# Kernel tuning notes

Measured on AMD Instinct MI355X. Metric: run time of the kernel, lower is better.

The kernel has to match this reference:

```python
import jax, jax.numpy as jnp
import numpy as np

N_NODES = 50000


def gcn_conv(x, W, b, src, dst, n_nodes):
    # PyG GCNConv: y = D^-1/2 (A + I) D^-1/2 (x @ W) + b, with D counting self-loops
    h = x @ W                                             # [N, out]
    deg = jnp.ones((n_nodes,), h.dtype).at[dst].add(1.0)  # in-degree + self-loop
    dinv = jax.lax.rsqrt(deg)
    norm = dinv[src] * dinv[dst]                          # [E]
    msg = h[src] * norm[:, None]                          # [E, out]
    out = jnp.zeros_like(h).at[dst].add(msg)              # scatter-add over edges
    out = out + h * (dinv * dinv)[:, None]                # self-loop contribution
    return out + b


def setup_inputs() -> dict:
    key = jax.random.key(0)
    k = jax.random.split(key, 7)
    d_in, d_hid, d_out = 128, 128, 64
    x = jax.random.normal(k[0], (N_NODES, d_in), jnp.float32)
    edge_index = jax.random.randint(k[1], (2, 800000), 0, N_NODES, jnp.int64)
    s1 = 1.0 / np.sqrt(d_in)
    s2 = 1.0 / np.sqrt(d_hid)
    W1 = jax.random.uniform(k[2], (d_in, d_hid), jnp.float32, -s1, s1)
    b1 = jnp.zeros((d_hid,), jnp.float32)
    W2 = jax.random.uniform(k[3], (d_hid, d_out), jnp.float32, -s2, s2)
    b2 = jnp.zeros((d_out,), jnp.float32)
    return {"x": x, "edge_index": edge_index, "W1": W1, "b1": b1, "W2": W2, "b2": b2}


def reference(x, edge_index, W1, b1, W2, b2):
    src, dst = edge_index[0], edge_index[1]
    h = jax.nn.relu(gcn_conv(x, W1, b1, src, dst, N_NODES))
    h = gcn_conv(h, W2, b2, src, dst, N_NODES)
    return jax.nn.log_softmax(h, axis=1)
```

## Files before the change

kernel.cpp:

```cpp
#include <hip/hip_runtime.h>
#include <hip/hip_bf16.h>
#include <math.h>


typedef unsigned int uint32;
typedef unsigned short ushort16;
typedef __attribute__((ext_vector_type(8))) short bf16x8;
typedef __attribute__((ext_vector_type(4))) float f32x4;

__device__ inline unsigned short f2bf_rne(float f) {
    uint32 x = __float_as_uint(f);
    uint32 r = (x + 0x7fffu + ((x >> 16) & 1u)) >> 16;
    return (unsigned short)r;
}
__device__ inline uint32 pack_bf16x2(float a, float b) {
    return (uint32)f2bf_rne(a) | ((uint32)f2bf_rne(b) << 16);
}
__device__ inline float2 unpack_bf16x2(uint32 u) {
    float2 r;
    r.x = __uint_as_float(u << 16);
    r.y = __uint_as_float(u & 0xffff0000u);
    return r;
}

#define NHB 128

__global__ __launch_bounds__(256) void hist_conv_k(const int* __restrict__ dst, int E,
                                                   int NW, int chunk,
                                                   uint32* __restrict__ counts_pb,
                                                   ushort16* __restrict__ rankx,
                                                   const float* __restrict__ W1,
                                                   const float* __restrict__ W2,
                                                   unsigned short* __restrict__ W1t,
                                                   unsigned short* __restrict__ W2t) {
    const int tid = threadIdx.x;
    if ((int)blockIdx.x >= 4 * NHB) {
        int idx = ((int)blockIdx.x - 4 * NHB) * 256 + tid;
        if (idx < 128 * 128) {
            int ns = idx >> 7, k = idx & 127;
            int t = ns >> 4, m = ns & 15;
            int col = 32 * (t >> 1) + 2 * m + (t & 1);
            W1t[idx] = f2bf_rne(W1[k * 128 + col]);
        } else {
            int i2 = idx - 128 * 128;
            if (i2 < 64 * 128) {
                int ns = i2 >> 7, k = i2 & 127;
                int t = ns >> 4, m = ns & 15;
                int col = 32 * (t >> 1) + 2 * m + (t & 1);
                W2t[i2] = f2bf_rne(W2[k * 64 + col]);
            }
        }
        return;
    }
    extern __shared__ uint32 sh[];
    const int hb  = blockIdx.x >> 2;
    const int qt  = blockIdx.x & 3;
    const int NWq = (NW + 3) >> 2;
    const int qlo = qt * NWq;
    const int qhi = min(NW, qlo + NWq);
    const int qn  = qhi - qlo;
    for (int i = tid; i < qn; i += 256) sh[i] = 0;
    __syncthreads();
    const int e0 = hb * chunk;
    const int e1 = min(E, e0 + chunk);
    int e = e0 + tid;
    for (; e + 768 < e1; e += 1024) {
        int d0 = dst[e];
        int d1 = dst[e + 256];
        int d2 = dst[e + 512];
        int d3 = dst[e + 768];
        int w0 = d0 >> 1, w1 = d1 >> 1, w2 = d2 >> 1, w3 = d3 >> 1;
        if (w0 >= qlo && w0 < qhi) {
            uint32 o = atomicAdd(&sh[w0 - qlo], (d0 & 1) ? 0x10000u : 1u);
            rankx[e] = (ushort16)((d0 & 1) ? (o >> 16) : (o & 0xffffu));
        }
        if (w1 >= qlo && w1 < qhi) {
            uint32 o = atomicAdd(&sh[w1 - qlo], (d1 & 1) ? 0x10000u : 1u);
            rankx[e + 256] = (ushort16)((d1 & 1) ? (o >> 16) : (o & 0xffffu));
        }
        if (w2 >= qlo && w2 < qhi) {
            uint32 o = atomicAdd(&sh[w2 - qlo], (d2 & 1) ? 0x10000u : 1u);
            rankx[e + 512] = (ushort16)((d2 & 1) ? (o >> 16) : (o & 0xffffu));
        }
        if (w3 >= qlo && w3 < qhi) {
            uint32 o = atomicAdd(&sh[w3 - qlo], (d3 & 1) ? 0x10000u : 1u);
            rankx[e + 768] = (ushort16)((d3 & 1) ? (o >> 16) : (o & 0xffffu));
        }
    }
    for (; e < e1; e += 256) {
        int d = dst[e];
        int w = d >> 1;
        if (w >= qlo && w < qhi) {
            uint32 o = atomicAdd(&sh[w - qlo], (d & 1) ? 0x10000u : 1u);
            rankx[e] = (ushort16)((d & 1) ? (o >> 16) : (o & 0xffffu));
        }
    }
    __syncthreads();
    uint32* dstp = counts_pb + (size_t)hb * NW + qlo;
    for (int i = tid; i < qn; i += 256) dstp[i] = sh[i];
}

__global__ __launch_bounds__(256) void scan2_k(const uint32* __restrict__ counts_pb,
                                               int N, int NW,
                                               ushort16* __restrict__ basecum,
                                               int* __restrict__ exscan,
                                               int* __restrict__ blocksum,
                                               float* __restrict__ dinv,
                                               ushort16* __restrict__ degs) {
    __shared__ int sd[256];
    const int tid = threadIdx.x;
    const int n   = blockIdx.x * 256 + tid;
    const int nc  = n < N ? n : N - 1;
    const int w   = nc >> 1;
    const bool hi = (nc & 1) != 0;
    int cum = 0;
    for (int bb = 0; bb < NHB; bb += 16) {
        uint32 wv[16];
#pragma unroll
        for (int j = 0; j < 16; ++j)
            wv[j] = counts_pb[(size_t)(bb + j) * NW + w];
#pragma unroll
        for (int j = 0; j < 16; ++j) {
            int c = hi ? (int)(wv[j] >> 16) : (int)(wv[j] & 0xffffu);
            if (n < N) basecum[(size_t)(bb + j) * N + n] = (ushort16)cum;
            cum += c;
        }
    }
    int v = (n < N) ? cum : 0;
    if (n < N) {
        dinv[n] = rsqrtf((float)(v + 1));
        degs[n] = (ushort16)v;
    }
    int vp = (v + 7) & ~7;
    sd[tid] = vp;
    __syncthreads();
    for (int off = 1; off < 256; off <<= 1) {
        int t = (tid >= off) ? sd[tid - off] : 0;
        __syncthreads();
        sd[tid] += t;
        __syncthreads();
    }
    if (n < N) exscan[n] = sd[tid] - vp;
    if (tid == 255) blocksum[blockIdx.x] = sd[255];
}

__global__ __launch_bounds__(256) void fill_gemm1_k(const int* __restrict__ src,
                                                    const int* __restrict__ dst, int E,
                                                    int chunk, int N,
                                                    const ushort16* __restrict__ rankx,
                                                    const ushort16* __restrict__ basecum,
                                                    const int* __restrict__ blocksum,
                                                    int NB,
                                                    const int* __restrict__ exscan,
                                                    const ushort16* __restrict__ degs,
                                                    int* __restrict__ offsets,
                                                    ushort16* __restrict__ csr_src,
                                                    const float* __restrict__ X,
                                                    const unsigned short* __restrict__ Wt,
                                                    const float* __restrict__ dinv,
                                                    uint32* __restrict__ Yu, int Nrows) {
    __shared__ int sd[256];
    __shared__ int ebs[256];
    __shared__ int total;
    if ((int)blockIdx.x < 256) {
        const int f   = blockIdx.x;
        const int tid = threadIdx.x;
        int v = (tid < NB) ? blocksum[tid] : 0;
        sd[tid] = v;
        __syncthreads();
        for (int off = 1; off < 256; off <<= 1) {
            int t = (tid >= off) ? sd[tid - off] : 0;
            __syncthreads();
            sd[tid] += t;
            __syncthreads();
        }
        ebs[tid] = sd[tid] - v;
        if (tid == 255) total = sd[255];
        __syncthreads();
        int g = f * 256 + tid;
        if (g < N) {
            int off = ebs[g >> 8] + exscan[g];
            offsets[g] = off;
            int dg = degs[g];
            int pl = (dg + 7) & ~7;
            for (int k = dg; k < pl; ++k) csr_src[off + k] = (ushort16)N;
        } else if (g == N) {
            offsets[N] = total;
        }
        const int b  = f >> 1;
        const ushort16* bc = basecum + (size_t)b * N;
        const int q2 = chunk >> 1;
        const int e0 = b * chunk + (f & 1) * q2;
        const int e1 = min(E, e0 + q2);
        int e = e0 + tid;
        for (; e + 768 < e1; e += 1024) {
#pragma unroll
            for (int j = 0; j < 4; ++j) {
                int ej = e + j * 256;
                int d = dst[ej];
                int pos = ebs[d >> 8] + exscan[d] + (int)bc[d] + (int)rankx[ej];
                csr_src[pos] = (ushort16)src[ej];
            }
        }
        for (; e < e1; e += 256) {
            int d = dst[e];
            int pos = ebs[d >> 8] + exscan[d] + (int)bc[d] + (int)rankx[e];
            csr_src[pos] = (ushort16)src[e];
        }
        return;
    }
    constexpr int NCOL = 128;
    constexpr int NT = NCOL / 16;
    const int tid  = threadIdx.x;
    const int wave = tid >> 6;
    const int lane = tid & 63;
    const int m16  = lane & 15;
    const int q    = lane >> 4;
    const int r0   = ((int)blockIdx.x - 256) * 64 + wave * 16;

    if ((int)blockIdx.x == 256 && tid < 64) Yu[(size_t)Nrows * (NCOL / 2) + tid] = 0;

    int arow = r0 + m16;
    if (arow >= Nrows) arow = Nrows - 1;

    bf16x8 afrag[4];
#pragma unroll
    for (int kb = 0; kb < 4; ++kb) {
        const float* p = &X[(size_t)arow * 128 + kb * 32 + q * 8];
        float4 u0 = *(const float4*)p;
        float4 u1 = *(const float4*)(p + 4);
        bf16x8 a;
        a[0] = (short)f2bf_rne(u0.x); a[1] = (short)f2bf_rne(u0.y);
        a[2] = (short)f2bf_rne(u0.z); a[3] = (short)f2bf_rne(u0.w);
        a[4] = (short)f2bf_rne(u1.x); a[5] = (short)f2bf_rne(u1.y);
        a[6] = (short)f2bf_rne(u1.z); a[7] = (short)f2bf_rne(u1.w);
        afrag[kb] = a;
    }

    f32x4 acc[NT];
#pragma unroll
    for (int t = 0; t < NT; ++t) acc[t] = (f32x4){0.f, 0.f, 0.f, 0.f};
#pragma unroll
    for (int t = 0; t < NT; ++t) {
        const unsigned short* Bp = &Wt[(size_t)(t * 16 + m16) * 128 + q * 8];
#pragma unroll
        for (int kb = 0; kb < 4; ++kb) {
            bf16x8 bfrag = *(const bf16x8*)&Bp[kb * 32];
            acc[t] = __builtin_amdgcn_mfma_f32_16x16x32_bf16(afrag[kb], bfrag, acc[t], 0, 0, 0);
        }
    }
#pragma unroll
    for (int i = 0; i < 4; ++i) {
        int row = r0 + q * 4 + i;
        if (row < Nrows) {
            float dn = dinv[row];
#pragma unroll
            for (int u = 0; u < NT / 2; ++u)
                Yu[(size_t)row * (NCOL / 2) + u * 16 + m16] =
                    pack_bf16x2(acc[2 * u][i] * dn, acc[2 * u + 1][i] * dn);
        }
    }
}

__global__ __launch_bounds__(256, 8) void agg1_gemm2_k(const unsigned short* __restrict__ hs,
                                                       const int* __restrict__ offsets,
                                                       const ushort16* __restrict__ csr_src,
                                                       const float* __restrict__ dinv,
                                                       const float* __restrict__ b1,
                                                       const unsigned short* __restrict__ W2t,
                                                       uint32* __restrict__ Yu, int N) {
    __shared__ uint32 srow[16 * 68];
    const int tid  = threadIdx.x;
    const int w    = tid >> 6;
    const int lane = tid & 63;
    const int base = (int)blockIdx.x * 16;
    const uint32* T = (const uint32*)hs;
    const float2 bb = ((const float2*)b1)[lane];
    if (blockIdx.x == 0 && w == 2 && lane < 32) Yu[(size_t)N * 32 + lane] = 0;
#pragma unroll
    for (int which = 0; which < 4; ++which) {
        const int node = base + 4 * w + which;
        uint32 packed = 0;
        if (node < N) {
            const int start = offsets[node];
            const int end   = offsets[node + 1];
            const float dn  = dinv[node];
            float2 self = unpack_bf16x2(T[(size_t)node * 64 + lane]);
            float ax0 = self.x, ay0 = self.y;
            float ax1 = 0.f, ay1 = 0.f, ax2 = 0.f, ay2 = 0.f, ax3 = 0.f, ay3 = 0.f;
            int p = start;
            for (; p + 15 < end; p += 16) {
                uint4 ia = *(const uint4*)&csr_src[p];
                uint4 ib = *(const uint4*)&csr_src[p + 8];
                int s0 = ia.x & 0xffff, s1 = ia.x >> 16;
                int s2 = ia.y & 0xffff, s3 = ia.y >> 16;
                int s4 = ia.z & 0xffff, s5 = ia.z >> 16;
                int s6 = ia.w & 0xffff, s7 = ia.w >> 16;
                int s8 = ib.x & 0xffff, s9 = ib.x >> 16;
                int sa = ib.y & 0xffff, sb = ib.y >> 16;
                int sc = ib.z & 0xffff, sd = ib.z >> 16;
                int se = ib.w & 0xffff, sf = ib.w >> 16;
                uint32 u0 = T[(size_t)s0 * 64 + lane];
                uint32 u1 = T[(size_t)s1 * 64 + lane];
                uint32 u2 = T[(size_t)s2 * 64 + lane];
                uint32 u3 = T[(size_t)s3 * 64 + lane];
                uint32 u4 = T[(size_t)s4 * 64 + lane];
                uint32 u5 = T[(size_t)s5 * 64 + lane];
                uint32 u6 = T[(size_t)s6 * 64 + lane];
                uint32 u7 = T[(size_t)s7 * 64 + lane];
                uint32 u8 = T[(size_t)s8 * 64 + lane];
                uint32 u9 = T[(size_t)s9 * 64 + lane];
                uint32 ua = T[(size_t)sa * 64 + lane];
                uint32 ub = T[(size_t)sb * 64 + lane];
                uint32 uc = T[(size_t)sc * 64 + lane];
                uint32 ud = T[(size_t)sd * 64 + lane];
                uint32 ue = T[(size_t)se * 64 + lane];
                uint32 uf = T[(size_t)sf * 64 + lane];
                float2 f0 = unpack_bf16x2(u0), f1 = unpack_bf16x2(u1);
                float2 f2 = unpack_bf16x2(u2), f3 = unpack_bf16x2(u3);
                float2 f4 = unpack_bf16x2(u4), f5 = unpack_bf16x2(u5);
                float2 f6 = unpack_bf16x2(u6), f7 = unpack_bf16x2(u7);
                float2 f8 = unpack_bf16x2(u8), f9 = unpack_bf16x2(u9);
                float2 fa = unpack_bf16x2(ua), fb = unpack_bf16x2(ub);
                float2 fc = unpack_bf16x2(uc), fd = unpack_bf16x2(ud);
                float2 fe = unpack_bf16x2(ue), ff = unpack_bf16x2(uf);
                ax0 += (f0.x + f4.x) + (f8.x + fc.x);
                ay0 += (f0.y + f4.y) + (f8.y + fc.y);
                ax1 += (f1.x + f5.x) + (f9.x + fd.x);
                ay1 += (f1.y + f5.y) + (f9.y + fd.y);
                ax2 += (f2.x + f6.x) + (fa.x + fe.x);
                ay2 += (f2.y + f6.y) + (fa.y + fe.y);
                ax3 += (f3.x + f7.x) + (fb.x + ff.x);
                ay3 += (f3.y + f7.y) + (fb.y + ff.y);
            }
            for (; p + 7 < end; p += 8) {
                uint4 ia = *(const uint4*)&csr_src[p];
                int s0 = ia.x & 0xffff, s1 = ia.x >> 16;
                int s2 = ia.y & 0xffff, s3 = ia.y >> 16;
                int s4 = ia.z & 0xffff, s5 = ia.z >> 16;
                int s6 = ia.w & 0xffff, s7 = ia.w >> 16;
                uint32 u0 = T[(size_t)s0 * 64 + lane];
                uint32 u1 = T[(size_t)s1 * 64 + lane];
                uint32 u2 = T[(size_t)s2 * 64 + lane];
                uint32 u3 = T[(size_t)s3 * 64 + lane];
                uint32 u4 = T[(size_t)s4 * 64 + lane];
                uint32 u5 = T[(size_t)s5 * 64 + lane];
                uint32 u6 = T[(size_t)s6 * 64 + lane];
                uint32 u7 = T[(size_t)s7 * 64 + lane];
                float2 f0 = unpack_bf16x2(u0), f1 = unpack_bf16x2(u1);
                float2 f2 = unpack_bf16x2(u2), f3 = unpack_bf16x2(u3);
                float2 f4 = unpack_bf16x2(u4), f5 = unpack_bf16x2(u5);
                float2 f6 = unpack_bf16x2(u6), f7 = unpack_bf16x2(u7);
                ax0 += f0.x + f4.x; ay0 += f0.y + f4.y;
                ax1 += f1.x + f5.x; ay1 += f1.y + f5.y;
                ax2 += f2.x + f6.x; ay2 += f2.y + f6.y;
                ax3 += f3.x + f7.x; ay3 += f3.y + f7.y;
            }
            float vx = ((ax0 + ax1) + (ax2 + ax3)) * dn + bb.x;
            float vy = ((ay0 + ay1) + (ay2 + ay3)) * dn + bb.y;
            vx = vx > 0.f ? vx : 0.f;
            vy = vy > 0.f ? vy : 0.f;
            packed = pack_bf16x2(vx, vy);
        }
        srow[(4 * w + which) * 68 + lane] = packed;
    }
    __syncthreads();
    if (w < 2) {
        const int pp  = w;
        const int m16 = lane & 15;
        const int q   = lane >> 4;
        bf16x8 afrag[4];
#pragma unroll
        for (int kb = 0; kb < 4; ++kb)
            afrag[kb] = *(const bf16x8*)&srow[m16 * 68 + kb * 16 + q * 4];
        f32x4 acc0 = (f32x4){0.f, 0.f, 0.f, 0.f};
        f32x4 acc1 = (f32x4){0.f, 0.f, 0.f, 0.f};
        const unsigned short* Bp0 = &W2t[(size_t)((2 * pp) * 16 + m16) * 128 + q * 8];
        const unsigned short* Bp1 = &W2t[(size_t)((2 * pp + 1) * 16 + m16) * 128 + q * 8];
#pragma unroll
        for (int kb = 0; kb < 4; ++kb) {
            bf16x8 b0  = *(const bf16x8*)&Bp0[kb * 32];
            bf16x8 b1f = *(const bf16x8*)&Bp1[kb * 32];
            acc0 = __builtin_amdgcn_mfma_f32_16x16x32_bf16(afrag[kb], b0, acc0, 0, 0, 0);
            acc1 = __builtin_amdgcn_mfma_f32_16x16x32_bf16(afrag[kb], b1f, acc1, 0, 0, 0);
        }
#pragma unroll
        for (int i = 0; i < 4; ++i) {
            int row = base + q * 4 + i;
            if (row < N) {
                float dn2 = dinv[row];
                Yu[(size_t)row * 32 + pp * 16 + m16] =
                    pack_bf16x2(acc0[i] * dn2, acc1[i] * dn2);
            }
        }
    }
}

__global__ __launch_bounds__(256, 8) void agg2_k(const unsigned short* __restrict__ hs,
                                                 const int* __restrict__ offsets,
                                                 const ushort16* __restrict__ csr_src,
                                                 const float* __restrict__ dinv,
                                                 const float* __restrict__ b2,
                                                 float* __restrict__ out, int N) {
    const int tid  = threadIdx.x;
    const int node = blockIdx.x * 8 + (tid >> 5);
    const int l    = tid & 31;
    if (node >= N) return;
    const uint32* T = (const uint32*)hs;
    const int start = offsets[node];
    const int end   = offsets[node + 1];
    const float dn  = dinv[node];
    float2 self = unpack_bf16x2(T[(size_t)node * 32 + l]);
    float ax0 = self.x, ay0 = self.y;
    float ax1 = 0.f, ay1 = 0.f, ax2 = 0.f, ay2 = 0.f, ax3 = 0.f, ay3 = 0.f;
    int p = start;
    for (; p + 15 < end; p += 16) {
        uint4 ia = *(const uint4*)&csr_src[p];
        uint4 ib = *(const uint4*)&csr_src[p + 8];
        int s0 = ia.x & 0xffff, s1 = ia.x >> 16;
        int s2 = ia.y & 0xffff, s3 = ia.y >> 16;
        int s4 = ia.z & 0xffff, s5 = ia.z >> 16;
        int s6 = ia.w & 0xffff, s7 = ia.w >> 16;
        int s8 = ib.x & 0xffff, s9 = ib.x >> 16;
        int sa = ib.y & 0xffff, sb = ib.y >> 16;
        int sc = ib.z & 0xffff, sd = ib.z >> 16;
        int se = ib.w & 0xffff, sf = ib.w >> 16;
        uint32 u0 = T[(size_t)s0 * 32 + l];
        uint32 u1 = T[(size_t)s1 * 32 + l];
        uint32 u2 = T[(size_t)s2 * 32 + l];
        uint32 u3 = T[(size_t)s3 * 32 + l];
        uint32 u4 = T[(size_t)s4 * 32 + l];
        uint32 u5 = T[(size_t)s5 * 32 + l];
        uint32 u6 = T[(size_t)s6 * 32 + l];
        uint32 u7 = T[(size_t)s7 * 32 + l];
        uint32 u8 = T[(size_t)s8 * 32 + l];
        uint32 u9 = T[(size_t)s9 * 32 + l];
        uint32 ua = T[(size_t)sa * 32 + l];
        uint32 ub = T[(size_t)sb * 32 + l];
        uint32 uc = T[(size_t)sc * 32 + l];
        uint32 ud = T[(size_t)sd * 32 + l];
        uint32 ue = T[(size_t)se * 32 + l];
        uint32 uf = T[(size_t)sf * 32 + l];
        float2 f0 = unpack_bf16x2(u0), f1 = unpack_bf16x2(u1);
        float2 f2 = unpack_bf16x2(u2), f3 = unpack_bf16x2(u3);
        float2 f4 = unpack_bf16x2(u4), f5 = unpack_bf16x2(u5);
        float2 f6 = unpack_bf16x2(u6), f7 = unpack_bf16x2(u7);
        float2 f8 = unpack_bf16x2(u8), f9 = unpack_bf16x2(u9);
        float2 fa = unpack_bf16x2(ua), fb = unpack_bf16x2(ub);
        float2 fc = unpack_bf16x2(uc), fd = unpack_bf16x2(ud);
        float2 fe = unpack_bf16x2(ue), ff = unpack_bf16x2(uf);
        ax0 += (f0.x + f4.x) + (f8.x + fc.x);
        ay0 += (f0.y + f4.y) + (f8.y + fc.y);
        ax1 += (f1.x + f5.x) + (f9.x + fd.x);
        ay1 += (f1.y + f5.y) + (f9.y + fd.y);
        ax2 += (f2.x + f6.x) + (fa.x + fe.x);
        ay2 += (f2.y + f6.y) + (fa.y + fe.y);
        ax3 += (f3.x + f7.x) + (fb.x + ff.x);
        ay3 += (f3.y + f7.y) + (fb.y + ff.y);
    }
    for (; p + 7 < end; p += 8) {
        uint4 ia = *(const uint4*)&csr_src[p];
        int s0 = ia.x & 0xffff, s1 = ia.x >> 16;
        int s2 = ia.y & 0xffff, s3 = ia.y >> 16;
        int s4 = ia.z & 0xffff, s5 = ia.z >> 16;
        int s6 = ia.w & 0xffff, s7 = ia.w >> 16;
        uint32 u0 = T[(size_t)s0 * 32 + l];
        uint32 u1 = T[(size_t)s1 * 32 + l];
        uint32 u2 = T[(size_t)s2 * 32 + l];
        uint32 u3 = T[(size_t)s3 * 32 + l];
        uint32 u4 = T[(size_t)s4 * 32 + l];
        uint32 u5 = T[(size_t)s5 * 32 + l];
        uint32 u6 = T[(size_t)s6 * 32 + l];
        uint32 u7 = T[(size_t)s7 * 32 + l];
        float2 f0 = unpack_bf16x2(u0), f1 = unpack_bf16x2(u1);
        float2 f2 = unpack_bf16x2(u2), f3 = unpack_bf16x2(u3);
        float2 f4 = unpack_bf16x2(u4), f5 = unpack_bf16x2(u5);
        float2 f6 = unpack_bf16x2(u6), f7 = unpack_bf16x2(u7);
        ax0 += f0.x + f4.x; ay0 += f0.y + f4.y;
        ax1 += f1.x + f5.x; ay1 += f1.y + f5.y;
        ax2 += f2.x + f6.x; ay2 += f2.y + f6.y;
        ax3 += f3.x + f7.x; ay3 += f3.y + f7.y;
    }
    float2 bb = ((const float2*)b2)[l];
    float vx = ((ax0 + ax1) + (ax2 + ax3)) * dn + bb.x;
    float vy = ((ay0 + ay1) + (ay2 + ay3)) * dn + bb.y;
    float m = fmaxf(vx, vy);
#pragma unroll
    for (int off = 16; off > 0; off >>= 1) m = fmaxf(m, __shfl_xor(m, off, 64));
    float ex = __expf(vx - m) + __expf(vy - m);
    float ssum = ex;
#pragma unroll
    for (int off = 16; off > 0; off >>= 1) ssum += __shfl_xor(ssum, off, 64);
    float lse = m + __logf(ssum);
    float2 o = {vx - lse, vy - lse};
    ((float2*)out)[(size_t)node * 32 + l] = o;
}

extern "C" void kernel_launch(void* const* d_in, const int* in_sizes, int n_in,
                              void* d_out, int out_size, void* d_ws, size_t ws_size,
                              hipStream_t stream) {
    const float* x  = (const float*)d_in[0];
    const int*   ei = (const int*)d_in[1];
    const float* W1 = (const float*)d_in[2];
    const float* b1 = (const float*)d_in[3];
    const float* W2 = (const float*)d_in[4];
    const float* b2 = (const float*)d_in[5];
    float* out = (float*)d_out;

    const int N = in_sizes[0] / 128;
    const int E = in_sizes[1] / 2;
    const int* src = ei;
    const int* dst = ei + E;
    const int NB = (N + 255) / 256;
    const int NW = (N + 1) / 2;
    const int NWq = (NW + 3) >> 2;
    const int chunk = (E + NHB - 1) / NHB;

    char* ws = (char*)d_ws;
    auto alloc = [&](size_t bytes) -> char* {
        char* p = ws;
        ws += (bytes + 255) & ~(size_t)255;
        return p;
    };
    unsigned short* h1  = (unsigned short*)alloc((size_t)(N + 1) * 128 * 2);
    unsigned short* h2  = (unsigned short*)alloc((size_t)(N + 1) * 64 * 2);
    uint32* counts_pb = (uint32*)alloc((size_t)NHB * NW * 4);
    ushort16* basecum = (ushort16*)alloc((size_t)NHB * N * 2);
    ushort16* rankx   = (ushort16*)alloc((size_t)E * 2);
    ushort16* csr_src = (ushort16*)alloc(((size_t)E + 8 * (size_t)N) * 2);
    float* dinv     = (float*)alloc((size_t)N * 4);
    int*   exscan   = (int*)alloc((size_t)N * 4);
    int*   blocksum = (int*)alloc((size_t)NB * 4);
    int*   offsets  = (int*)alloc((size_t)(N + 1) * 4);
    ushort16* degs  = (ushort16*)alloc((size_t)N * 2);
    unsigned short* W1t = (unsigned short*)alloc(128 * 128 * 2);
    unsigned short* W2t = (unsigned short*)alloc(64 * 128 * 2);

    const int GB = (N + 63) / 64;
    const int CB = (128 * 128 + 64 * 128 + 255) / 256;

    hist_conv_k<<<4 * NHB + CB, 256, NWq * 4, stream>>>(dst, E, NW, chunk, counts_pb,
                                                        rankx, W1, W2, W1t, W2t);
    scan2_k<<<NB, 256, 0, stream>>>(counts_pb, N, NW, basecum, exscan, blocksum, dinv,
                                    degs);
    fill_gemm1_k<<<256 + GB, 256, 0, stream>>>(src, dst, E, chunk, N, rankx, basecum,
                                               blocksum, NB, exscan, degs, offsets,
                                               csr_src, x, W1t, dinv, (uint32*)h1, N);
    agg1_gemm2_k<<<(N + 15) / 16, 256, 0, stream>>>(h1, offsets, csr_src, dinv, b1,
                                                    W2t, (uint32*)h2, N);
    agg2_k<<<(N + 7) / 8, 256, 0, stream>>>(h2, offsets, csr_src, dinv, b2, out, N);
}
```

Before: 180.0 us.

## Pack CSR-build counters into 8-bit fields and split agg2 edges across half-waves

The histogram now packs four 8-bit per-node counters into each shared-memory word instead of two 16-bit ones. This shrinks counts_pb, and stores rankx and basecum as bytes, which cuts memory traffic in the hist, scan and fill kernels. The final aggregation kernel now gives each node a full 64-lane wave and splits its edge list between the two 32-lane halves, combining them with a shuffle. This adds parallelism per node but drops the 16-wide unrolled path. The 8-bit counters assume that per-node degree, and its running sum across histogram blocks, stays below 256; larger degrees would overflow silently.

```diff
diff --git a/kernel.cpp b/kernel.cpp
--- a/kernel.cpp
+++ b/kernel.cpp
@@ -5,6 +5,7 @@
 
 typedef unsigned int uint32;
 typedef unsigned short ushort16;
+typedef unsigned char uchar;
 typedef __attribute__((ext_vector_type(8))) short bf16x8;
 typedef __attribute__((ext_vector_type(4))) float f32x4;
 
@@ -26,9 +27,9 @@
 #define NHB 128
 
 __global__ __launch_bounds__(256) void hist_conv_k(const int* __restrict__ dst, int E,
-                                                   int NW, int chunk,
+                                                   int NWb, int chunk,
                                                    uint32* __restrict__ counts_pb,
-                                                   ushort16* __restrict__ rankx,
+                                                   uchar* __restrict__ rankx,
                                                    const float* __restrict__ W1,
                                                    const float* __restrict__ W2,
                                                    unsigned short* __restrict__ W1t,
@@ -55,9 +56,9 @@
     extern __shared__ uint32 sh[];
     const int hb  = blockIdx.x >> 2;
     const int qt  = blockIdx.x & 3;
-    const int NWq = (NW + 3) >> 2;
+    const int NWq = (NWb + 3) >> 2;
     const int qlo = qt * NWq;
-    const int qhi = min(NW, qlo + NWq);
+    const int qhi = min(NWb, qlo + NWq);
     const int qn  = qhi - qlo;
     for (int i = tid; i < qn; i += 256) sh[i] = 0;
     __syncthreads();
@@ -69,40 +70,40 @@
         int d1 = dst[e + 256];
         int d2 = dst[e + 512];
         int d3 = dst[e + 768];
-        int w0 = d0 >> 1, w1 = d1 >> 1, w2 = d2 >> 1, w3 = d3 >> 1;
+        int w0 = d0 >> 2, w1 = d1 >> 2, w2 = d2 >> 2, w3 = d3 >> 2;
         if (w0 >= qlo && w0 < qhi) {
-            uint32 o = atomicAdd(&sh[w0 - qlo], (d0 & 1) ? 0x10000u : 1u);
-            rankx[e] = (ushort16)((d0 & 1) ? (o >> 16) : (o & 0xffffu));
+            uint32 o = atomicAdd(&sh[w0 - qlo], 1u << (8 * (d0 & 3)));
+            rankx[e] = (uchar)(o >> (8 * (d0 & 3)));
         }
         if (w1 >= qlo && w1 < qhi) {
-            uint32 o = atomicAdd(&sh[w1 - qlo], (d1 & 1) ? 0x10000u : 1u);
-            rankx[e + 256] = (ushort16)((d1 & 1) ? (o >> 16) : (o & 0xffffu));
+            uint32 o = atomicAdd(&sh[w1 - qlo], 1u << (8 * (d1 & 3)));
+            rankx[e + 256] = (uchar)(o >> (8 * (d1 & 3)));
         }
         if (w2 >= qlo && w2 < qhi) {
-            uint32 o = atomicAdd(&sh[w2 - qlo], (d2 & 1) ? 0x10000u : 1u);
-            rankx[e + 512] = (ushort16)((d2 & 1) ? (o >> 16) : (o & 0xffffu));
+            uint32 o = atomicAdd(&sh[w2 - qlo], 1u << (8 * (d2 & 3)));
+            rankx[e + 512] = (uchar)(o >> (8 * (d2 & 3)));
         }
         if (w3 >= qlo && w3 < qhi) {
-            uint32 o = atomicAdd(&sh[w3 - qlo], (d3 & 1) ? 0x10000u : 1u);
-            rankx[e + 768] = (ushort16)((d3 & 1) ? (o >> 16) : (o & 0xffffu));
+            uint32 o = atomicAdd(&sh[w3 - qlo], 1u << (8 * (d3 & 3)));
+            rankx[e + 768] = (uchar)(o >> (8 * (d3 & 3)));
         }
     }
     for (; e < e1; e += 256) {
         int d = dst[e];
-        int w = d >> 1;
+        int w = d >> 2;
         if (w >= qlo && w < qhi) {
-            uint32 o = atomicAdd(&sh[w - qlo], (d & 1) ? 0x10000u : 1u);
-            rankx[e] = (ushort16)((d & 1) ? (o >> 16) : (o & 0xffffu));
+            uint32 o = atomicAdd(&sh[w - qlo], 1u << (8 * (d & 3)));
+            rankx[e] = (uchar)(o >> (8 * (d & 3)));
         }
     }
     __syncthreads();
-    uint32* dstp = counts_pb + (size_t)hb * NW + qlo;
+    uint32* dstp = counts_pb + (size_t)hb * NWb + qlo;
     for (int i = tid; i < qn; i += 256) dstp[i] = sh[i];
 }
 
 __global__ __launch_bounds__(256) void scan2_k(const uint32* __restrict__ counts_pb,
-                                               int N, int NW,
-                                               ushort16* __restrict__ basecum,
+                                               int N, int NWb,
+                                               uchar* __restrict__ basecum,
                                                int* __restrict__ exscan,
                                                int* __restrict__ blocksum,
                                                float* __restrict__ dinv,
@@ -111,18 +112,18 @@
     const int tid = threadIdx.x;
     const int n   = blockIdx.x * 256 + tid;
     const int nc  = n < N ? n : N - 1;
-    const int w   = nc >> 1;
-    const bool hi = (nc & 1) != 0;
+    const int wq  = nc >> 2;
+    const int sh8 = 8 * (nc & 3);
     int cum = 0;
     for (int bb = 0; bb < NHB; bb += 16) {
         uint32 wv[16];
 #pragma unroll
         for (int j = 0; j < 16; ++j)
-            wv[j] = counts_pb[(size_t)(bb + j) * NW + w];
+            wv[j] = counts_pb[(size_t)(bb + j) * NWb + wq];
 #pragma unroll
         for (int j = 0; j < 16; ++j) {
-            int c = hi ? (int)(wv[j] >> 16) : (int)(wv[j] & 0xffffu);
-            if (n < N) basecum[(size_t)(bb + j) * N + n] = (ushort16)cum;
+            int c = (int)((wv[j] >> sh8) & 0xffu);
+            if (n < N) basecum[(size_t)(bb + j) * N + n] = (uchar)cum;
             cum += c;
         }
     }
@@ -147,8 +148,8 @@
 __global__ __launch_bounds__(256) void fill_gemm1_k(const int* __restrict__ src,
                                                     const int* __restrict__ dst, int E,
                                                     int chunk, int N,
-                                                    const ushort16* __restrict__ rankx,
-                                                    const ushort16* __restrict__ basecum,
+                                                    const uchar* __restrict__ rankx,
+                                                    const uchar* __restrict__ basecum,
                                                     const int* __restrict__ blocksum,
                                                     int NB,
                                                     const int* __restrict__ exscan,
@@ -188,7 +189,7 @@
             offsets[N] = total;
         }
         const int b  = f >> 1;
-        const ushort16* bc = basecum + (size_t)b * N;
+        const uchar* bc = basecum + (size_t)b * N;
         const int q2 = chunk >> 1;
         const int e0 = b * chunk + (f & 1) * q2;
         const int e1 = min(E, e0 + q2);
@@ -403,62 +404,23 @@
                                                  const float* __restrict__ b2,
                                                  float* __restrict__ out, int N) {
     const int tid  = threadIdx.x;
-    const int node = blockIdx.x * 8 + (tid >> 5);
-    const int l    = tid & 31;
+    const int w    = tid >> 6;
+    const int lane = tid & 63;
+    const int half = lane >> 5;
+    const int l    = lane & 31;
+    const int node = blockIdx.x * 4 + w;
     if (node >= N) return;
     const uint32* T = (const uint32*)hs;
     const int start = offsets[node];
     const int end   = offsets[node + 1];
     const float dn  = dinv[node];
-    float2 self = unpack_bf16x2(T[(size_t)node * 32 + l]);
-    float ax0 = self.x, ay0 = self.y;
+    float ax0 = 0.f, ay0 = 0.f;
+    if (half == 0) {
+        float2 self = unpack_bf16x2(T[(size_t)node * 32 + l]);
+        ax0 = self.x; ay0 = self.y;
+    }
     float ax1 = 0.f, ay1 = 0.f, ax2 = 0.f, ay2 = 0.f, ax3 = 0.f, ay3 = 0.f;
-    int p = start;
-    for (; p + 15 < end; p += 16) {
-        uint4 ia = *(const uint4*)&csr_src[p];
-        uint4 ib = *(const uint4*)&csr_src[p + 8];
-        int s0 = ia.x & 0xffff, s1 = ia.x >> 16;
-        int s2 = ia.y & 0xffff, s3 = ia.y >> 16;
-        int s4 = ia.z & 0xffff, s5 = ia.z >> 16;
-        int s6 = ia.w & 0xffff, s7 = ia.w >> 16;
-        int s8 = ib.x & 0xffff, s9 = ib.x >> 16;
-        int sa = ib.y & 0xffff, sb = ib.y >> 16;
-        int sc = ib.z & 0xffff, sd = ib.z >> 16;
-        int se = ib.w & 0xffff, sf = ib.w >> 16;
-        uint32 u0 = T[(size_t)s0 * 32 + l];
-        uint32 u1 = T[(size_t)s1 * 32 + l];
-        uint32 u2 = T[(size_t)s2 * 32 + l];
-        uint32 u3 = T[(size_t)s3 * 32 + l];
-        uint32 u4 = T[(size_t)s4 * 32 + l];
-        uint32 u5 = T[(size_t)s5 * 32 + l];
-        uint32 u6 = T[(size_t)s6 * 32 + l];
-        uint32 u7 = T[(size_t)s7 * 32 + l];
-        uint32 u8 = T[(size_t)s8 * 32 + l];
-        uint32 u9 = T[(size_t)s9 * 32 + l];
-        uint32 ua = T[(size_t)sa * 32 + l];
-        uint32 ub = T[(size_t)sb * 32 + l];
-        uint32 uc = T[(size_t)sc * 32 + l];
-        uint32 ud = T[(size_t)sd * 32 + l];
-        uint32 ue = T[(size_t)se * 32 + l];
-        uint32 uf = T[(size_t)sf * 32 + l];
-        float2 f0 = unpack_bf16x2(u0), f1 = unpack_bf16x2(u1);
-        float2 f2 = unpack_bf16x2(u2), f3 = unpack_bf16x2(u3);
-        float2 f4 = unpack_bf16x2(u4), f5 = unpack_bf16x2(u5);
-        float2 f6 = unpack_bf16x2(u6), f7 = unpack_bf16x2(u7);
-        float2 f8 = unpack_bf16x2(u8), f9 = unpack_bf16x2(u9);
-        float2 fa = unpack_bf16x2(ua), fb = unpack_bf16x2(ub);
-        float2 fc = unpack_bf16x2(uc), fd = unpack_bf16x2(ud);
-        float2 fe = unpack_bf16x2(ue), ff = unpack_bf16x2(uf);
-        ax0 += (f0.x + f4.x) + (f8.x + fc.x);
-        ay0 += (f0.y + f4.y) + (f8.y + fc.y);
-        ax1 += (f1.x + f5.x) + (f9.x + fd.x);
-        ay1 += (f1.y + f5.y) + (f9.y + fd.y);
-        ax2 += (f2.x + f6.x) + (fa.x + fe.x);
-        ay2 += (f2.y + f6.y) + (fa.y + fe.y);
-        ax3 += (f3.x + f7.x) + (fb.x + ff.x);
-        ay3 += (f3.y + f7.y) + (fb.y + ff.y);
-    }
-    for (; p + 7 < end; p += 8) {
+    for (int p = start + half * 8; p < end; p += 16) {
         uint4 ia = *(const uint4*)&csr_src[p];
         int s0 = ia.x & 0xffff, s1 = ia.x >> 16;
         int s2 = ia.y & 0xffff, s3 = ia.y >> 16;
@@ -481,9 +443,13 @@
         ax2 += f2.x + f6.x; ay2 += f2.y + f6.y;
         ax3 += f3.x + f7.x; ay3 += f3.y + f7.y;
     }
+    float sx = (ax0 + ax1) + (ax2 + ax3);
+    float sy = (ay0 + ay1) + (ay2 + ay3);
+    sx += __shfl_xor(sx, 32, 64);
+    sy += __shfl_xor(sy, 32, 64);
     float2 bb = ((const float2*)b2)[l];
-    float vx = ((ax0 + ax1) + (ax2 + ax3)) * dn + bb.x;
-    float vy = ((ay0 + ay1) + (ay2 + ay3)) * dn + bb.y;
+    float vx = sx * dn + bb.x;
+    float vy = sy * dn + bb.y;
     float m = fmaxf(vx, vy);
 #pragma unroll
     for (int off = 16; off > 0; off >>= 1) m = fmaxf(m, __shfl_xor(m, off, 64));
@@ -492,8 +458,10 @@
 #pragma unroll
     for (int off = 16; off > 0; off >>= 1) ssum += __shfl_xor(ssum, off, 64);
     float lse = m + __logf(ssum);
-    float2 o = {vx - lse, vy - lse};
-    ((float2*)out)[(size_t)node * 32 + l] = o;
+    if (half == 0) {
+        float2 o = {vx - lse, vy - lse};
+        ((float2*)out)[(size_t)node * 32 + l] = o;
+    }
 }
 
 extern "C" void kernel_launch(void* const* d_in, const int* in_sizes, int n_in,
@@ -512,8 +480,8 @@
     const int* src = ei;
     const int* dst = ei + E;
     const int NB = (N + 255) / 256;
-    const int NW = (N + 1) / 2;
-    const int NWq = (NW + 3) >> 2;
+    const int NWb = (N + 3) / 4;
+    const int NWq = (NWb + 3) >> 2;
     const int chunk = (E + NHB - 1) / NHB;
 
     char* ws = (char*)d_ws;
@@ -524,9 +492,9 @@
     };
     unsigned short* h1  = (unsigned short*)alloc((size_t)(N + 1) * 128 * 2);
     unsigned short* h2  = (unsigned short*)alloc((size_t)(N + 1) * 64 * 2);
-    uint32* counts_pb = (uint32*)alloc((size_t)NHB * NW * 4);
-    ushort16* basecum = (ushort16*)alloc((size_t)NHB * N * 2);
-    ushort16* rankx   = (ushort16*)alloc((size_t)E * 2);
+    uint32* counts_pb = (uint32*)alloc((size_t)NHB * NWb * 4);
+    uchar* basecum  = (uchar*)alloc((size_t)NHB * N);
+    uchar* rankx    = (uchar*)alloc((size_t)E);
     ushort16* csr_src = (ushort16*)alloc(((size_t)E + 8 * (size_t)N) * 2);
     float* dinv     = (float*)alloc((size_t)N * 4);
     int*   exscan   = (int*)alloc((size_t)N * 4);
@@ -539,14 +507,14 @@
     const int GB = (N + 63) / 64;
     const int CB = (128 * 128 + 64 * 128 + 255) / 256;
 
-    hist_conv_k<<<4 * NHB + CB, 256, NWq * 4, stream>>>(dst, E, NW, chunk, counts_pb,
+    hist_conv_k<<<4 * NHB + CB, 256, NWq * 4, stream>>>(dst, E, NWb, chunk, counts_pb,
                                                         rankx, W1, W2, W1t, W2t);
-    scan2_k<<<NB, 256, 0, stream>>>(counts_pb, N, NW, basecum, exscan, blocksum, dinv,
+    scan2_k<<<NB, 256, 0, stream>>>(counts_pb, N, NWb, basecum, exscan, blocksum, dinv,
                                     degs);
     fill_gemm1_k<<<256 + GB, 256, 0, stream>>>(src, dst, E, chunk, N, rankx, basecum,
                                                blocksum, NB, exscan, degs, offsets,
                                                csr_src, x, W1t, dinv, (uint32*)h1, N);
     agg1_gemm2_k<<<(N + 15) / 16, 256, 0, stream>>>(h1, offsets, csr_src, dinv, b1,
                                                     W2t, (uint32*)h2, N);
-    agg2_k<<<(N + 7) / 8, 256, 0, stream>>>(h2, offsets, csr_src, dinv, b2, out, N);
-}
+    agg2_k<<<(N + 3) / 4, 256, 0, stream>>>(h2, offsets, csr_src, dinv, b2, out, N);
+}
```

New measurement: 186.2 us. +3.4%, slower.
